# Optimization experiments

Hardware: AMD Instinct MI355X
Metric: run time of the kernel (lower is better)

## Reference

```python
import jax, jax.numpy as jnp
import numpy as np

# config dims (see shape_source)
NO = 8        # Max_Object
NT = 32       # Max_Time
C = 512       # feat_dims
VD = 1024     # visual_dim
RD = 300      # self.nfeat (relation word-vector dim)
H = 4         # headnum
B = 8         # batch
No = NT * 2 * NO      # 512 object-graph nodes
Nr = NT * NO * NO     # 2048 relation-graph nodes


def _glorot(key, shape):
    fan_in = shape[0]
    return jax.random.normal(key, shape, dtype=jnp.float32) / np.sqrt(fan_in)


def setup_inputs() -> dict:
    key = jax.random.key(0)
    ks = jax.random.split(key, 18)
    inp = {
        "Ao": jax.random.uniform(ks[0], (B, No, No), dtype=jnp.float32),
        "srco": jax.random.normal(ks[1], (B, 1, 1, No, VD), dtype=jnp.float32),
        "Ar": jax.random.uniform(ks[2], (B, Nr, Nr), dtype=jnp.float32),
        "srcr": jax.random.normal(ks[3], (B, 1, 1, Nr, RD), dtype=jnp.float32),
        # GraphConvolution weights: gcl_o/gcl2_o and gcl_r/gcl2_r
        "Wo1": _glorot(ks[4], (VD, 1024)),
        "Wo2": _glorot(ks[5], (1024, C)),
        "Wr1": _glorot(ks[6], (RD, 1024)),
        "Wr2": _glorot(ks[7], (1024, C)),
        # MultiHeadAttention (e2n) projections
        "Wq": _glorot(ks[8], (C, C)), "bq": jnp.zeros((C,), jnp.float32),
        "Wk": _glorot(ks[9], (C, C)), "bk": jnp.zeros((C,), jnp.float32),
        "Wv": _glorot(ks[10], (C, C)), "bv": jnp.zeros((C,), jnp.float32),
        "Wp": _glorot(ks[11], (C, C)), "bp": jnp.zeros((C,), jnp.float32),
        # e2n_embed: Linear(2C -> C)
        "We": _glorot(ks[12], (2 * C, C)), "be": jnp.zeros((C,), jnp.float32),
    }
    return inp


def _gcn2(A, x, W1, W2):
    """Two stacked GraphConvolution layers with self-loops: relu((A+I) @ x @ W).
    A: (b,N,N), x: (b,N,Din). Vectorized over batch (torch code loops per-sample)."""
    eye = jnp.eye(A.shape[-1], dtype=A.dtype)
    Ah = A + eye
    h = jax.nn.relu(jnp.einsum('bij,bjd->bid', Ah, x @ W1))
    return jax.nn.relu(jnp.einsum('bij,bjd->bid', Ah, h @ W2))


def _mha(x, Wq, bq, Wk, bk, Wv, bv, Wp, bp):
    """Standard multi-head self-attention. x: (Bseg, S, C)."""
    Bs, S, _ = x.shape
    dh = C // H
    q = (x @ Wq + bq).reshape(Bs, S, H, dh)
    k = (x @ Wk + bk).reshape(Bs, S, H, dh)
    v = (x @ Wv + bv).reshape(Bs, S, H, dh)
    attn = jax.nn.softmax(jnp.einsum('bqhd,bkhd->bhqk', q, k) / np.sqrt(dh), axis=-1)
    o = jnp.einsum('bhqk,bkhd->bqhd', attn, v).reshape(Bs, S, C)
    return o @ Wp + bp


def _forward(Ao, srco, Ar, srcr, Wo1, Wo2, Wr1, Wr2,
             Wq, bq, Wk, bk, Wv, bv, Wp, bp, We, be):
    b = Ao.shape[0]
    # object-graph GCN (torch loops over batch; vectorized here)
    xo = srco[:, 0, 0, :, :VD]                       # (b, No, VD)
    srco_gcn = _gcn2(Ao, xo, Wo1, Wo2)               # (b, No, C)
    out_gcn_o = srco_gcn.reshape(b, NT, 2 * NO, C)
    # relation-graph GCN
    xr = srcr[:, 0, 0]                               # (b, Nr, RD)
    srcr_gcn = _gcn2(Ar, xr, Wr1, Wr2)               # (b, Nr, C)
    out_gcn_r = srcr_gcn.reshape(b, NT, NO * NO, C)
    # compute_e2n: segment-wise MHA over NO-token windows (torch loops over NO)
    r = out_gcn_r.reshape(b * NT, NO, NO, C)
    seg_a = r.reshape(b * NT * NO, NO, C)                      # rows of NOxNO grid
    a = _mha(seg_a, Wq, bq, Wk, bk, Wv, bv, Wp, bp).mean(axis=1)
    a = a.reshape(b * NT, NO, C)
    seg_o = jnp.swapaxes(r, 1, 2).reshape(b * NT * NO, NO, C)  # cols (permute 0,2,1,3)
    o = _mha(seg_o, Wq, bq, Wk, bk, Wv, bv, Wp, bp).mean(axis=1)
    o = o.reshape(b * NT, NO, C)
    tmp = jnp.concatenate([a, o], axis=1)                      # (b*NT, 2*NO, C)
    cat = jnp.concatenate([tmp, out_gcn_o.reshape(b * NT, 2 * NO, C)], axis=-1)
    out_e2n = cat @ We + be
    return out_e2n.reshape(b, NT, 2 * NO, C)


def reference(Ao, srco, Ar, srcr, Wo1, Wo2, Wr1, Wr2,
              Wq, bq, Wk, bk, Wv, bv, Wp, bp, We, be):
    return _forward(Ao, srco, Ar, srcr, Wo1, Wo2, Wr1, Wr2,
                    Wq, bq, Wk, bk, Wv, bv, Wp, bp, We, be)
```

## Files before the change

### kernel.cpp

```cpp
#include <hip/hip_runtime.h>
#include <hip/hip_bf16.h>


typedef __attribute__((ext_vector_type(4))) float f32x4;
typedef __attribute__((ext_vector_type(8))) short bf16x8s;

#define TILE 128
#define BKK 32
#define LDSS 40

__device__ inline void splt(float v, unsigned short& h, unsigned short& l) {
    __hip_bfloat16 hb = __float2bfloat16(v);
    float hf = __bfloat162float(hb);
    __hip_bfloat16 lb = __float2bfloat16(v - hf);
    h = *(unsigned short*)&hb;
    l = *(unsigned short*)&lb;
}

__global__ __launch_bounds__(256) void gemm3p(
    const __hip_bfloat16* __restrict__ AH, const __hip_bfloat16* __restrict__ AL,
    long long sA, int lda,
    const __hip_bfloat16* __restrict__ BTH, const __hip_bfloat16* __restrict__ BTL,
    long long sBT, int ldbt,
    float* __restrict__ DF,
    __hip_bfloat16* __restrict__ DH, __hip_bfloat16* __restrict__ DL,
    long long sD, int ldd,
    const __hip_bfloat16* __restrict__ addNH, const __hip_bfloat16* __restrict__ addNL,
    long long sAddN, int ldaddN,
    const __hip_bfloat16* __restrict__ addTH, const __hip_bfloat16* __restrict__ addTL,
    long long sAddT, int ldaddT,
    const float* __restrict__ bias,
    int K, int relu)
{
    __shared__ __hip_bfloat16 Ahs[TILE * LDSS], Als[TILE * LDSS];
    __shared__ __hip_bfloat16 Bhs[TILE * LDSS], Bls[TILE * LDSS];

    const int tid  = threadIdx.x;
    const int lane = tid & 63;
    const int wave = tid >> 6;
    const int wm   = (wave >> 1) * 64;
    const int wn   = (wave & 1) * 64;
    const int row0 = blockIdx.y * TILE;
    const int col0 = blockIdx.x * TILE;
    const int b    = blockIdx.z;

    const __hip_bfloat16* AHb = AH + (size_t)b * sA;
    const __hip_bfloat16* ALb = AL + (size_t)b * sA;
    const __hip_bfloat16* BHb = BTH + (size_t)b * sBT;
    const __hip_bfloat16* BLb = BTL + (size_t)b * sBT;

    f32x4 acc[4][4];
#pragma unroll
    for (int i = 0; i < 4; ++i)
#pragma unroll
        for (int j = 0; j < 4; ++j) acc[i][j] = (f32x4){0.f, 0.f, 0.f, 0.f};

    const int quad = lane >> 4;
    const int l16  = lane & 15;

    for (int k0 = 0; k0 < K; k0 += BKK) {
        __syncthreads();
#pragma unroll
        for (int it = 0; it < 2; ++it) {
            int task = tid + it * 256;
            int m = task >> 2, kq = task & 3;
            size_t go = (size_t)(row0 + m) * lda + k0 + kq * 8;
            *(uint4*)(&Ahs[m * LDSS + kq * 8]) = *(const uint4*)(AHb + go);
            *(uint4*)(&Als[m * LDSS + kq * 8]) = *(const uint4*)(ALb + go);
        }
#pragma unroll
        for (int it = 0; it < 2; ++it) {
            int task = tid + it * 256;
            int n = task >> 2, kq = task & 3;
            size_t go = (size_t)(col0 + n) * ldbt + k0 + kq * 8;
            *(uint4*)(&Bhs[n * LDSS + kq * 8]) = *(const uint4*)(BHb + go);
            *(uint4*)(&Bls[n * LDSS + kq * 8]) = *(const uint4*)(BLb + go);
        }
        __syncthreads();

        bf16x8s ah[4], al[4], bh[4], bl[4];
#pragma unroll
        for (int mt = 0; mt < 4; ++mt) {
            int r = (wm + mt * 16 + l16) * LDSS + quad * 8;
            ah[mt] = *(const bf16x8s*)(&Ahs[r]);
            al[mt] = *(const bf16x8s*)(&Als[r]);
        }
#pragma unroll
        for (int nt = 0; nt < 4; ++nt) {
            int r = (wn + nt * 16 + l16) * LDSS + quad * 8;
            bh[nt] = *(const bf16x8s*)(&Bhs[r]);
            bl[nt] = *(const bf16x8s*)(&Bls[r]);
        }
#pragma unroll
        for (int mt = 0; mt < 4; ++mt)
#pragma unroll
            for (int nt = 0; nt < 4; ++nt) {
                acc[mt][nt] = __builtin_amdgcn_mfma_f32_16x16x32_bf16(ah[mt], bh[nt], acc[mt][nt], 0, 0, 0);
                acc[mt][nt] = __builtin_amdgcn_mfma_f32_16x16x32_bf16(ah[mt], bl[nt], acc[mt][nt], 0, 0, 0);
                acc[mt][nt] = __builtin_amdgcn_mfma_f32_16x16x32_bf16(al[mt], bh[nt], acc[mt][nt], 0, 0, 0);
            }
    }

    float* DFb = DF ? DF + (size_t)b * sD : nullptr;
    __hip_bfloat16* DHb = DH ? DH + (size_t)b * sD : nullptr;
    __hip_bfloat16* DLb = DL ? DL + (size_t)b * sD : nullptr;
    const __hip_bfloat16* aNH = addNH ? addNH + (size_t)b * sAddN : nullptr;
    const __hip_bfloat16* aNL = addNL ? addNL + (size_t)b * sAddN : nullptr;
    const __hip_bfloat16* aTH = addTH ? addTH + (size_t)b * sAddT : nullptr;
    const __hip_bfloat16* aTL = addTL ? addTL + (size_t)b * sAddT : nullptr;
#pragma unroll
    for (int mt = 0; mt < 4; ++mt)
#pragma unroll
        for (int nt = 0; nt < 4; ++nt)
#pragma unroll
            for (int r = 0; r < 4; ++r) {
                int m = row0 + wm + mt * 16 + quad * 4 + r;
                int n = col0 + wn + nt * 16 + l16;
                float v = acc[mt][nt][r];
                if (aNH) v += __bfloat162float(aNH[(size_t)m * ldaddN + n])
                            + __bfloat162float(aNL[(size_t)m * ldaddN + n]);
                if (aTH) v += __bfloat162float(aTH[(size_t)n * ldaddT + m])
                            + __bfloat162float(aTL[(size_t)n * ldaddT + m]);
                if (bias) v += bias[n];
                if (relu && v < 0.f) v = 0.f;
                if (DFb) DFb[(size_t)m * ldd + n] = v;
                else {
                    unsigned short h, l;
                    splt(v, h, l);
                    ((unsigned short*)DHb)[(size_t)m * ldd + n] = h;
                    ((unsigned short*)DLb)[(size_t)m * ldd + n] = l;
                }
            }
}

__global__ void split_planes(const float* __restrict__ src,
                             __hip_bfloat16* __restrict__ H,
                             __hip_bfloat16* __restrict__ L, int n8)
{
    int i = blockIdx.x * blockDim.x + threadIdx.x;
    if (i >= n8) return;
    float4 v0 = ((const float4*)src)[i * 2];
    float4 v1 = ((const float4*)src)[i * 2 + 1];
    float vals[8] = {v0.x, v0.y, v0.z, v0.w, v1.x, v1.y, v1.z, v1.w};
    unsigned short hh[8], ll[8];
#pragma unroll
    for (int u = 0; u < 8; ++u) splt(vals[u], hh[u], ll[u]);
    *(uint4*)((unsigned short*)H + (size_t)i * 8) = *(uint4*)hh;
    *(uint4*)((unsigned short*)L + (size_t)i * 8) = *(uint4*)ll;
}

__global__ __launch_bounds__(256) void padtrans_split(
    const float* __restrict__ src, __hip_bfloat16* __restrict__ dH,
    __hip_bfloat16* __restrict__ dL, int R, int C, int Rp, int Cp)
{
    __shared__ float T[64][65];
    const int t = threadIdx.x;
    const int tr = t >> 4, tc = t & 15;
    const int c0 = blockIdx.x * 64, r0 = blockIdx.y * 64;
    const size_t bat = blockIdx.z;
    const float* sb = src + bat * (size_t)R * C;
    unsigned short* dHb = (unsigned short*)dH + bat * (size_t)Cp * Rp;
    unsigned short* dLb = (unsigned short*)dL + bat * (size_t)Cp * Rp;

#pragma unroll
    for (int i = 0; i < 4; ++i) {
        int rr = tr + i * 16;
        int gr = r0 + rr;
        float v0 = 0.f, v1 = 0.f, v2 = 0.f, v3 = 0.f;
        if (gr < R) {
            int c = c0 + tc * 4;
            const float* s = sb + (size_t)gr * C + c;
            if (c + 0 < C) v0 = s[0];
            if (c + 1 < C) v1 = s[1];
            if (c + 2 < C) v2 = s[2];
            if (c + 3 < C) v3 = s[3];
        }
        T[rr][tc * 4 + 0] = v0; T[rr][tc * 4 + 1] = v1;
        T[rr][tc * 4 + 2] = v2; T[rr][tc * 4 + 3] = v3;
    }
    __syncthreads();
#pragma unroll
    for (int i = 0; i < 4; ++i) {
        int cc = tr + i * 16;
        unsigned short h[4], l[4];
#pragma unroll
        for (int u = 0; u < 4; ++u) splt(T[tc * 4 + u][cc], h[u], l[u]);
        size_t off = (size_t)(c0 + cc) * Rp + r0 + tc * 4;
        *(ushort4*)(dHb + off) = *(ushort4*)h;
        *(ushort4*)(dLb + off) = *(ushort4*)l;
    }
}

__global__ __launch_bounds__(256) void trans_bf16(
    const __hip_bfloat16* __restrict__ sH, const __hip_bfloat16* __restrict__ sL,
    __hip_bfloat16* __restrict__ dH, __hip_bfloat16* __restrict__ dL,
    int R, int C)
{
    __shared__ unsigned short T[64][68];
    const int plane = blockIdx.z & 1;
    const size_t bat = blockIdx.z >> 1;
    const unsigned short* s = (const unsigned short*)(plane ? sL : sH) + bat * (size_t)R * C;
    unsigned short* d = (unsigned short*)(plane ? dL : dH) + bat * (size_t)R * C;
    const int t = threadIdx.x;
    const int tr = t >> 4, tc = t & 15;
    const int c0 = blockIdx.x * 64, r0 = blockIdx.y * 64;
#pragma unroll
    for (int i = 0; i < 4; ++i) {
        int rr = tr + i * 16;
        ushort4 v = *(const ushort4*)(s + (size_t)(r0 + rr) * C + c0 + tc * 4);
        T[rr][tc * 4 + 0] = v.x; T[rr][tc * 4 + 1] = v.y;
        T[rr][tc * 4 + 2] = v.z; T[rr][tc * 4 + 3] = v.w;
    }
    __syncthreads();
#pragma unroll
    for (int i = 0; i < 4; ++i) {
        int cc = tr + i * 16;
        ushort4 o = { T[tc * 4 + 0][cc], T[tc * 4 + 1][cc],
                      T[tc * 4 + 2][cc], T[tc * 4 + 3][cc] };
        *(ushort4*)(d + (size_t)(c0 + cc) * R + r0 + tc * 4) = o;
    }
}

__global__ __launch_bounds__(256) void gemm_bf16(
    const __hip_bfloat16* __restrict__ A, long long sA, int lda,
    const __hip_bfloat16* __restrict__ B, long long sB, int ldb,
    void* __restrict__ D, long long sD, int ldd,
    const __hip_bfloat16* __restrict__ addsrc, long long sAdd, int ldadd,
    const float* __restrict__ bias,
    int K, int relu, int outF32)
{
    __shared__ __hip_bfloat16 As[TILE * LDSS];
    __shared__ __hip_bfloat16 Bs[TILE * LDSS];

    const int tid  = threadIdx.x;
    const int lane = tid & 63;
    const int wave = tid >> 6;
    const int wm   = (wave >> 1) * 64;
    const int wn   = (wave & 1) * 64;
    const int row0 = blockIdx.y * TILE;
    const int col0 = blockIdx.x * TILE;
    const int b    = blockIdx.z;

    const __hip_bfloat16* Ab = A + (size_t)b * sA;
    const __hip_bfloat16* Bb = B + (size_t)b * sB;

    f32x4 acc[4][4];
#pragma unroll
    for (int i = 0; i < 4; ++i)
#pragma unroll
        for (int j = 0; j < 4; ++j) acc[i][j] = (f32x4){0.f, 0.f, 0.f, 0.f};

    const int quad = lane >> 4;
    const int l16  = lane & 15;

    for (int k0 = 0; k0 < K; k0 += BKK) {
        __syncthreads();
#pragma unroll
        for (int it = 0; it < 2; ++it) {
            int task = tid + it * 256;
            int m = task >> 2, kq = task & 3;
            uint4 val = *(const uint4*)(Ab + (size_t)(row0 + m) * lda + k0 + kq * 8);
            *(uint4*)(&As[m * LDSS + kq * 8]) = val;
        }
#pragma unroll
        for (int it = 0; it < 2; ++it) {
            int task = tid + it * 256;
            int kk = task >> 4, n8 = task & 15;
            uint4 val = *(const uint4*)(Bb + (size_t)(k0 + kk) * ldb + col0 + n8 * 8);
            const __hip_bfloat16* v16 = (const __hip_bfloat16*)&val;
#pragma unroll
            for (int u = 0; u < 8; ++u)
                Bs[(n8 * 8 + u) * LDSS + kk] = v16[u];
        }
        __syncthreads();

        bf16x8s afrag[4], bfrag[4];
#pragma unroll
        for (int mt = 0; mt < 4; ++mt)
            afrag[mt] = *(const bf16x8s*)(&As[(wm + mt * 16 + l16) * LDSS + quad * 8]);
#pragma unroll
        for (int nt = 0; nt < 4; ++nt)
            bfrag[nt] = *(const bf16x8s*)(&Bs[(wn + nt * 16 + l16) * LDSS + quad * 8]);
#pragma unroll
        for (int mt = 0; mt < 4; ++mt)
#pragma unroll
            for (int nt = 0; nt < 4; ++nt)
                acc[mt][nt] = __builtin_amdgcn_mfma_f32_16x16x32_bf16(
                    afrag[mt], bfrag[nt], acc[mt][nt], 0, 0, 0);
    }

    __hip_bfloat16* Db16 = (__hip_bfloat16*)D + (size_t)b * sD;
    float*          DbF  = (float*)D + (size_t)b * sD;
    const __hip_bfloat16* Addb = addsrc ? addsrc + (size_t)b * sAdd : nullptr;
#pragma unroll
    for (int mt = 0; mt < 4; ++mt)
#pragma unroll
        for (int nt = 0; nt < 4; ++nt)
#pragma unroll
            for (int r = 0; r < 4; ++r) {
                int m = row0 + wm + mt * 16 + quad * 4 + r;
                int n = col0 + wn + nt * 16 + l16;
                float v = acc[mt][nt][r];
                if (Addb) v += __bfloat162float(Addb[(size_t)m * ldadd + n]);
                if (bias) v += bias[n];
                if (relu && v < 0.f) v = 0.f;
                if (outF32) DbF[(size_t)m * ldd + n] = v;
                else        Db16[(size_t)m * ldd + n] = __float2bfloat16(v);
            }
}

__global__ void convert_kernel(const float* __restrict__ src,
                               __hip_bfloat16* __restrict__ dst, int n4)
{
    int i = blockIdx.x * blockDim.x + threadIdx.x;
    if (i >= n4) return;
    float4 v = ((const float4*)src)[i];
    __hip_bfloat16 t0 = __float2bfloat16(v.x), t1 = __float2bfloat16(v.y);
    __hip_bfloat16 t2 = __float2bfloat16(v.z), t3 = __float2bfloat16(v.w);
    ushort4 o = { *(unsigned short*)&t0, *(unsigned short*)&t1,
                  *(unsigned short*)&t2, *(unsigned short*)&t3 };
    ((ushort4*)dst)[i] = o;
}

__global__ __launch_bounds__(256) void attn_kernel(
    const float* __restrict__ q,
    const float* __restrict__ k,
    const float* __restrict__ v,
    __hip_bfloat16* __restrict__ abar)
{
    __shared__ float qs[8][512], ks[8][512], vs[8][512];
    __shared__ float sc[4][8][8];
    __shared__ float wb[4][8];

    const int tid  = threadIdx.x;
    const int mode = blockIdx.y;
    const int g    = blockIdx.x >> 3;
    const int idx  = blockIdx.x & 7;
    const int rowBase = g * 64;

    for (int t = tid; t < 512; t += 256) {
        int p = t >> 6, c8 = (t & 63) * 8;
        int row = (mode == 0) ? (rowBase + idx * 8 + p) : (rowBase + p * 8 + idx);
        const float* qp = q + (size_t)row * 512 + c8;
        const float* kp = k + (size_t)row * 512 + c8;
        const float* vp = v + (size_t)row * 512 + c8;
        *(float4*)(&qs[p][c8])     = *(const float4*)(qp);
        *(float4*)(&qs[p][c8 + 4]) = *(const float4*)(qp + 4);
        *(float4*)(&ks[p][c8])     = *(const float4*)(kp);
        *(float4*)(&ks[p][c8 + 4]) = *(const float4*)(kp + 4);
        *(float4*)(&vs[p][c8])     = *(const float4*)(vp);
        *(float4*)(&vs[p][c8 + 4]) = *(const float4*)(vp + 4);
    }
    __syncthreads();

    {
        int h = tid >> 6, l = tid & 63;
        int i = l >> 3, j = l & 7;
        const float* qrow = &qs[i][h * 128];
        const float* krow = &ks[j][h * 128];
        float s = 0.f;
#pragma unroll
        for (int d = 0; d < 128; d += 4) {
            float4 qa = *(const float4*)(qrow + d);
            float4 kb = *(const float4*)(krow + d);
            s += qa.x * kb.x + qa.y * kb.y + qa.z * kb.z + qa.w * kb.w;
        }
        sc[h][i][j] = s * 0.08838834764831845f;
    }
    __syncthreads();

    if (tid < 32) {
        int h = tid >> 3, i = tid & 7;
        float mx = -1e30f;
#pragma unroll
        for (int j = 0; j < 8; ++j) mx = fmaxf(mx, sc[h][i][j]);
        float e[8], sum = 0.f;
#pragma unroll
        for (int j = 0; j < 8; ++j) { e[j] = __expf(sc[h][i][j] - mx); sum += e[j]; }
        float inv = 1.f / sum;
#pragma unroll
        for (int j = 0; j < 8; ++j) sc[h][i][j] = e[j] * inv;
    }
    __syncthreads();

    if (tid < 32) {
        int h = tid >> 3, j = tid & 7;
        float s = 0.f;
#pragma unroll
        for (int i = 0; i < 8; ++i) s += sc[h][i][j];
        wb[h][j] = s * 0.125f;
    }
    __syncthreads();

    {
        int orow = g * 16 + mode * 8 + idx;
        for (int c = tid; c < 512; c += 256) {
            int h = c >> 7;
            float o = 0.f;
#pragma unroll
            for (int j = 0; j < 8; ++j) o += wb[h][j] * vs[j][c];
            abar[(size_t)orow * 512 + c] = __float2bfloat16(o);
        }
    }
}


extern "C" void kernel_launch(void* const* d_in, const int* in_sizes, int n_in,
                              void* d_out, int out_size, void* d_ws, size_t ws_size,
                              hipStream_t stream)
{
    const float* Ao   = (const float*)d_in[0];
    const float* srco = (const float*)d_in[1];
    const float* Ar   = (const float*)d_in[2];
    const float* srcr = (const float*)d_in[3];
    const float* Wo1  = (const float*)d_in[4];
    const float* Wo2  = (const float*)d_in[5];
    const float* Wr1  = (const float*)d_in[6];
    const float* Wr2  = (const float*)d_in[7];
    const float* Wq   = (const float*)d_in[8];
    const float* bq   = (const float*)d_in[9];
    const float* Wk   = (const float*)d_in[10];
    const float* bk   = (const float*)d_in[11];
    const float* Wv   = (const float*)d_in[12];
    const float* bv   = (const float*)d_in[13];
    const float* Wp   = (const float*)d_in[14];
    const float* bp   = (const float*)d_in[15];
    const float* We   = (const float*)d_in[16];
    const float* be   = (const float*)d_in[17];
    float* out = (float*)d_out;

    char* ws = (char*)d_ws;
    __hip_bfloat16* ArH   = (__hip_bfloat16*)(ws + 0);
    __hip_bfloat16* ArL   = (__hip_bfloat16*)(ws + 67108864);
    __hip_bfloat16* XPTH  = (__hip_bfloat16*)(ws + 134217728);
    __hip_bfloat16* XPTL  = (__hip_bfloat16*)(ws + 146800640);
    __hip_bfloat16* UH    = (__hip_bfloat16*)(ws + 159383552);
    __hip_bfloat16* UL    = (__hip_bfloat16*)(ws + 171966464);
    __hip_bfloat16* HRH   = (__hip_bfloat16*)(ws + 184549376);
    __hip_bfloat16* HRL   = (__hip_bfloat16*)(ws + 218103808);
    __hip_bfloat16* T2RH  = (__hip_bfloat16*)(ws + 134217728);
    __hip_bfloat16* T2RL  = (__hip_bfloat16*)(ws + 150994944);
    __hip_bfloat16* T2RTH = (__hip_bfloat16*)(ws + 167772160);
    __hip_bfloat16* T2RTL = (__hip_bfloat16*)(ws + 184549376);
    __hip_bfloat16* GRH   = (__hip_bfloat16*)(ws + 201326592);
    __hip_bfloat16* GRL   = (__hip_bfloat16*)(ws + 218103808);
    float* qF = (float*)(ws + 0);
    float* kF = (float*)(ws + 33554432);
    float* vF = (float*)(ws + 67108864);
    __hip_bfloat16* ABAR  = (__hip_bfloat16*)(ws + 100663296);
    __hip_bfloat16* TO    = (__hip_bfloat16*)(ws + 104857600);
    __hip_bfloat16* HO    = (__hip_bfloat16*)(ws + 113246208);
    __hip_bfloat16* T2O   = (__hip_bfloat16*)(ws + 121634816);
    __hip_bfloat16* CAT   = (__hip_bfloat16*)(ws + 125829120);
    __hip_bfloat16* srcoB = (__hip_bfloat16*)(ws + 134217728);
    __hip_bfloat16* AoB   = (__hip_bfloat16*)(ws + 142606336);
    __hip_bfloat16* Wo1B  = (__hip_bfloat16*)(ws + 146800640);
    __hip_bfloat16* Wo2B  = (__hip_bfloat16*)(ws + 148897792);
    __hip_bfloat16* WeB   = (__hip_bfloat16*)(ws + 149946368);
    __hip_bfloat16* WpB   = (__hip_bfloat16*)(ws + 150994944);
    __hip_bfloat16* WPTH  = (__hip_bfloat16*)(ws + 251658240);
    __hip_bfloat16* WPTL  = (__hip_bfloat16*)(ws + 252313600);
    __hip_bfloat16* Wr2TH = (__hip_bfloat16*)(ws + 252968960);
    __hip_bfloat16* Wr2TL = (__hip_bfloat16*)(ws + 254017536);
    __hip_bfloat16* WqTH  = (__hip_bfloat16*)(ws + 255066112);
    __hip_bfloat16* WqTL  = (__hip_bfloat16*)(ws + 255590400);
    __hip_bfloat16* WkTH  = (__hip_bfloat16*)(ws + 256114688);
    __hip_bfloat16* WkTL  = (__hip_bfloat16*)(ws + 256638976);
    __hip_bfloat16* WvB   = (__hip_bfloat16*)(ws + 257163264);

    dim3 blk(256);
    auto cvt = [&](const float* s, __hip_bfloat16* d, int n) {
        convert_kernel<<<dim3((n / 4 + 255) / 256), blk, 0, stream>>>(s, d, n / 4);
    };

    split_planes<<<dim3(33554432 / 8 / 256), blk, 0, stream>>>(Ar, ArH, ArL, 33554432 / 8);
    padtrans_split<<<dim3(6, 32, 8), blk, 0, stream>>>(srcr, XPTH, XPTL, 2048, 300, 2048, 384);
    padtrans_split<<<dim3(16, 5, 1), blk, 0, stream>>>(Wr1, WPTH, WPTL, 300, 1024, 320, 1024);
    padtrans_split<<<dim3(8, 16, 1), blk, 0, stream>>>(Wr2, Wr2TH, Wr2TL, 1024, 512, 1024, 512);
    padtrans_split<<<dim3(8, 8, 1), blk, 0, stream>>>(Wq, WqTH, WqTL, 512, 512, 512, 512);
    padtrans_split<<<dim3(8, 8, 1), blk, 0, stream>>>(Wk, WkTH, WkTL, 512, 512, 512, 512);
    cvt(Wv, WvB, 262144);

    gemm3p<<<dim3(3, 16, 8), blk, 0, stream>>>(
        ArH, ArL, 2048LL * 2048, 2048, XPTH, XPTL, 384LL * 2048, 2048,
        nullptr, UH, UL, 2048LL * 384, 384,
        nullptr, nullptr, 0, 0, XPTH, XPTL, 384LL * 2048, 2048,
        nullptr, 2048, 0);
    gemm3p<<<dim3(8, 128, 1), blk, 0, stream>>>(
        UH, UL, 0, 384, WPTH, WPTL, 0, 320,
        nullptr, HRH, HRL, 0, 1024,
        nullptr, nullptr, 0, 0, nullptr, nullptr, 0, 0,
        nullptr, 320, 1);
    gemm3p<<<dim3(4, 128, 1), blk, 0, stream>>>(
        HRH, HRL, 0, 1024, Wr2TH, Wr2TL, 0, 1024,
        nullptr, T2RH, T2RL, 0, 512,
        nullptr, nullptr, 0, 0, nullptr, nullptr, 0, 0,
        nullptr, 1024, 0);
    trans_bf16<<<dim3(8, 32, 16), blk, 0, stream>>>(T2RH, T2RL, T2RTH, T2RTL, 2048, 512);
    gemm3p<<<dim3(4, 16, 8), blk, 0, stream>>>(
        ArH, ArL, 2048LL * 2048, 2048, T2RTH, T2RTL, 512LL * 2048, 2048,
        nullptr, GRH, GRL, 2048LL * 512, 512,
        T2RH, T2RL, 2048LL * 512, 512, nullptr, nullptr, 0, 0,
        nullptr, 2048, 1);
    gemm3p<<<dim3(4, 128, 1), blk, 0, stream>>>(
        GRH, GRL, 0, 512, WqTH, WqTL, 0, 512,
        qF, nullptr, nullptr, 0, 512,
        nullptr, nullptr, 0, 0, nullptr, nullptr, 0, 0,
        bq, 512, 0);
    gemm3p<<<dim3(4, 128, 1), blk, 0, stream>>>(
        GRH, GRL, 0, 512, WkTH, WkTL, 0, 512,
        kF, nullptr, nullptr, 0, 512,
        nullptr, nullptr, 0, 0, nullptr, nullptr, 0, 0,
        bk, 512, 0);
    gemm_bf16<<<dim3(4, 128, 1), blk, 0, stream>>>(
        GRH, 0, 512, WvB, 0, 512, vF, 0, 512,
        nullptr, 0, 0, bv, 512, 0, 1);
    attn_kernel<<<dim3(2048, 2), blk, 0, stream>>>(qF, kF, vF, ABAR);

    cvt(srco, srcoB, 4194304);
    cvt(Ao, AoB, 2097152);
    cvt(Wo1, Wo1B, 1048576);
    cvt(Wo2, Wo2B, 524288);
    cvt(We, WeB, 524288);
    cvt(Wp, WpB, 262144);
    gemm_bf16<<<dim3(8, 32, 1), blk, 0, stream>>>(srcoB, 0, 1024, Wo1B, 0, 1024,
        TO, 0, 1024, nullptr, 0, 0, nullptr, 1024, 0, 0);
    gemm_bf16<<<dim3(8, 4, 8), blk, 0, stream>>>(AoB, 512LL * 512, 512, TO, 512LL * 1024, 1024,
        HO, 512LL * 1024, 1024, TO, 512LL * 1024, 1024, nullptr, 512, 1, 0);
    gemm_bf16<<<dim3(4, 32, 1), blk, 0, stream>>>(HO, 0, 1024, Wo2B, 0, 512,
        T2O, 0, 512, nullptr, 0, 0, nullptr, 1024, 0, 0);
    gemm_bf16<<<dim3(4, 4, 8), blk, 0, stream>>>(AoB, 512LL * 512, 512, T2O, 512LL * 512, 512,
        (void*)(CAT + 512), 512LL * 1024, 1024, T2O, 512LL * 512, 512, nullptr, 512, 1, 0);
    gemm_bf16<<<dim3(4, 32, 1), blk, 0, stream>>>(ABAR, 0, 512, WpB, 0, 512,
        CAT, 0, 1024, nullptr, 0, 0, bp, 512, 0, 0);
    gemm_bf16<<<dim3(4, 32, 1), blk, 0, stream>>>(CAT, 0, 1024, WeB, 0, 512,
        out, 0, 512, nullptr, 0, 0, be, 1024, 0, 1);
}
```

Measured before the change: 1.258 ms.

## Double-buffer LDS tiles in GEMM kernels and fuse Q/K projections

Both GEMM kernels now use two LDS buffers and prefetch the next K-slice from global memory into registers while the current slice's MFMAs run, leaving one barrier per iteration instead of two. Separately, the Q and K projection weights are packed into one 1024-wide transposed matrix, so a single gemm3p launch writes an interleaved QK buffer using a per-column bias select, and the attention kernel reads Q and K from that buffer. The cost is doubled LDS use, which may lower occupancy, and more live registers for the prefetch.

```diff
diff --git a/kernel.cpp b/kernel.cpp
--- a/kernel.cpp
+++ b/kernel.cpp
@@ -29,11 +29,11 @@
     long long sAddN, int ldaddN,
     const __hip_bfloat16* __restrict__ addTH, const __hip_bfloat16* __restrict__ addTL,
     long long sAddT, int ldaddT,
-    const float* __restrict__ bias,
+    const float* __restrict__ bias, const float* __restrict__ bias2, int nsplit,
     int K, int relu)
 {
-    __shared__ __hip_bfloat16 Ahs[TILE * LDSS], Als[TILE * LDSS];
-    __shared__ __hip_bfloat16 Bhs[TILE * LDSS], Bls[TILE * LDSS];
+    __shared__ __hip_bfloat16 Ahs[2][TILE * LDSS], Als[2][TILE * LDSS];
+    __shared__ __hip_bfloat16 Bhs[2][TILE * LDSS], Bls[2][TILE * LDSS];
 
     const int tid  = threadIdx.x;
     const int lane = tid & 63;
@@ -49,6 +49,9 @@
     const __hip_bfloat16* BHb = BTH + (size_t)b * sBT;
     const __hip_bfloat16* BLb = BTL + (size_t)b * sBT;
 
+    const int mA  = tid >> 2;
+    const int kqA = (tid & 3) * 8;
+
     f32x4 acc[4][4];
 #pragma unroll
     for (int i = 0; i < 4; ++i)
@@ -58,38 +61,50 @@
     const int quad = lane >> 4;
     const int l16  = lane & 15;
 
+    {
+#pragma unroll
+        for (int it = 0; it < 2; ++it) {
+            int m = mA + it * 64;
+            size_t goA = (size_t)(row0 + m) * lda + kqA;
+            size_t goB = (size_t)(col0 + m) * ldbt + kqA;
+            int lo = m * LDSS + kqA;
+            *(uint4*)(&Ahs[0][lo]) = *(const uint4*)(AHb + goA);
+            *(uint4*)(&Als[0][lo]) = *(const uint4*)(ALb + goA);
+            *(uint4*)(&Bhs[0][lo]) = *(const uint4*)(BHb + goB);
+            *(uint4*)(&Bls[0][lo]) = *(const uint4*)(BLb + goB);
+        }
+    }
+    __syncthreads();
+
+    int cur = 0;
     for (int k0 = 0; k0 < K; k0 += BKK) {
-        __syncthreads();
-#pragma unroll
-        for (int it = 0; it < 2; ++it) {
-            int task = tid + it * 256;
-            int m = task >> 2, kq = task & 3;
-            size_t go = (size_t)(row0 + m) * lda + k0 + kq * 8;
-            *(uint4*)(&Ahs[m * LDSS + kq * 8]) = *(const uint4*)(AHb + go);
-            *(uint4*)(&Als[m * LDSS + kq * 8]) = *(const uint4*)(ALb + go);
-        }
-#pragma unroll
-        for (int it = 0; it < 2; ++it) {
-            int task = tid + it * 256;
-            int n = task >> 2, kq = task & 3;
-            size_t go = (size_t)(col0 + n) * ldbt + k0 + kq * 8;
-            *(uint4*)(&Bhs[n * LDSS + kq * 8]) = *(const uint4*)(BHb + go);
-            *(uint4*)(&Bls[n * LDSS + kq * 8]) = *(const uint4*)(BLb + go);
-        }
-        __syncthreads();
+        const bool pf = (k0 + BKK) < K;
+        uint4 rAH[2], rAL[2], rBH[2], rBL[2];
+        if (pf) {
+#pragma unroll
+            for (int it = 0; it < 2; ++it) {
+                int m = mA + it * 64;
+                size_t goA = (size_t)(row0 + m) * lda + (k0 + BKK) + kqA;
+                size_t goB = (size_t)(col0 + m) * ldbt + (k0 + BKK) + kqA;
+                rAH[it] = *(const uint4*)(AHb + goA);
+                rAL[it] = *(const uint4*)(ALb + goA);
+                rBH[it] = *(const uint4*)(BHb + goB);
+                rBL[it] = *(const uint4*)(BLb + goB);
+            }
+        }
 
         bf16x8s ah[4], al[4], bh[4], bl[4];
 #pragma unroll
         for (int mt = 0; mt < 4; ++mt) {
             int r = (wm + mt * 16 + l16) * LDSS + quad * 8;
-            ah[mt] = *(const bf16x8s*)(&Ahs[r]);
-            al[mt] = *(const bf16x8s*)(&Als[r]);
+            ah[mt] = *(const bf16x8s*)(&Ahs[cur][r]);
+            al[mt] = *(const bf16x8s*)(&Als[cur][r]);
         }
 #pragma unroll
         for (int nt = 0; nt < 4; ++nt) {
             int r = (wn + nt * 16 + l16) * LDSS + quad * 8;
-            bh[nt] = *(const bf16x8s*)(&Bhs[r]);
-            bl[nt] = *(const bf16x8s*)(&Bls[r]);
+            bh[nt] = *(const bf16x8s*)(&Bhs[cur][r]);
+            bl[nt] = *(const bf16x8s*)(&Bls[cur][r]);
         }
 #pragma unroll
         for (int mt = 0; mt < 4; ++mt)
@@ -99,6 +114,21 @@
                 acc[mt][nt] = __builtin_amdgcn_mfma_f32_16x16x32_bf16(ah[mt], bl[nt], acc[mt][nt], 0, 0, 0);
                 acc[mt][nt] = __builtin_amdgcn_mfma_f32_16x16x32_bf16(al[mt], bh[nt], acc[mt][nt], 0, 0, 0);
             }
+
+        if (pf) {
+            int nxt = cur ^ 1;
+#pragma unroll
+            for (int it = 0; it < 2; ++it) {
+                int m = mA + it * 64;
+                int lo = m * LDSS + kqA;
+                *(uint4*)(&Ahs[nxt][lo]) = rAH[it];
+                *(uint4*)(&Als[nxt][lo]) = rAL[it];
+                *(uint4*)(&Bhs[nxt][lo]) = rBH[it];
+                *(uint4*)(&Bls[nxt][lo]) = rBL[it];
+            }
+        }
+        __syncthreads();
+        cur ^= 1;
     }
 
     float* DFb = DF ? DF + (size_t)b * sD : nullptr;
@@ -121,7 +151,7 @@
                             + __bfloat162float(aNL[(size_t)m * ldaddN + n]);
                 if (aTH) v += __bfloat162float(aTH[(size_t)n * ldaddT + m])
                             + __bfloat162float(aTL[(size_t)n * ldaddT + m]);
-                if (bias) v += bias[n];
+                if (bias) v += (bias2 && n >= nsplit) ? bias2[n - nsplit] : bias[n];
                 if (relu && v < 0.f) v = 0.f;
                 if (DFb) DFb[(size_t)m * ldd + n] = v;
                 else {
@@ -229,8 +259,8 @@
     const float* __restrict__ bias,
     int K, int relu, int outF32)
 {
-    __shared__ __hip_bfloat16 As[TILE * LDSS];
-    __shared__ __hip_bfloat16 Bs[TILE * LDSS];
+    __shared__ __hip_bfloat16 As[2][TILE * LDSS];
+    __shared__ __hip_bfloat16 Bs[2][TILE * LDSS];
 
     const int tid  = threadIdx.x;
     const int lane = tid & 63;
@@ -244,6 +274,11 @@
     const __hip_bfloat16* Ab = A + (size_t)b * sA;
     const __hip_bfloat16* Bb = B + (size_t)b * sB;
 
+    const int mA  = tid >> 2;
+    const int kqA = (tid & 3) * 8;
+    const int kkB = tid >> 4;
+    const int n8B = (tid & 15) * 8;
+
     f32x4 acc[4][4];
 #pragma unroll
     for (int i = 0; i < 4; ++i)
@@ -253,40 +288,65 @@
     const int quad = lane >> 4;
     const int l16  = lane & 15;
 
+    {
+#pragma unroll
+        for (int it = 0; it < 2; ++it) {
+            int m = mA + it * 64;
+            *(uint4*)(&As[0][m * LDSS + kqA]) =
+                *(const uint4*)(Ab + (size_t)(row0 + m) * lda + kqA);
+            int kk = kkB + it * 16;
+            uint4 val = *(const uint4*)(Bb + (size_t)kk * ldb + col0 + n8B);
+            const __hip_bfloat16* v16 = (const __hip_bfloat16*)&val;
+#pragma unroll
+            for (int u = 0; u < 8; ++u)
+                Bs[0][(n8B + u) * LDSS + kk] = v16[u];
+        }
+    }
+    __syncthreads();
+
+    int cur = 0;
     for (int k0 = 0; k0 < K; k0 += BKK) {
-        __syncthreads();
-#pragma unroll
-        for (int it = 0; it < 2; ++it) {
-            int task = tid + it * 256;
-            int m = task >> 2, kq = task & 3;
-            uint4 val = *(const uint4*)(Ab + (size_t)(row0 + m) * lda + k0 + kq * 8);
-            *(uint4*)(&As[m * LDSS + kq * 8]) = val;
-        }
-#pragma unroll
-        for (int it = 0; it < 2; ++it) {
-            int task = tid + it * 256;
-            int kk = task >> 4, n8 = task & 15;
-            uint4 val = *(const uint4*)(Bb + (size_t)(k0 + kk) * ldb + col0 + n8 * 8);
-            const __hip_bfloat16* v16 = (const __hip_bfloat16*)&val;
-#pragma unroll
-            for (int u = 0; u < 8; ++u)
-                Bs[(n8 * 8 + u) * LDSS + kk] = v16[u];
-        }
-        __syncthreads();
+        const bool pf = (k0 + BKK) < K;
+        uint4 rA[2], rB[2];
+        if (pf) {
+#pragma unroll
+            for (int it = 0; it < 2; ++it) {
+                int m = mA + it * 64;
+                rA[it] = *(const uint4*)(Ab + (size_t)(row0 + m) * lda + (k0 + BKK) + kqA);
+                int kk = kkB + it * 16;
+                rB[it] = *(const uint4*)(Bb + (size_t)(k0 + BKK + kk) * ldb + col0 + n8B);
+            }
+        }
 
         bf16x8s afrag[4], bfrag[4];
 #pragma unroll
         for (int mt = 0; mt < 4; ++mt)
-            afrag[mt] = *(const bf16x8s*)(&As[(wm + mt * 16 + l16) * LDSS + quad * 8]);
+            afrag[mt] = *(const bf16x8s*)(&As[cur][(wm + mt * 16 + l16) * LDSS + quad * 8]);
 #pragma unroll
         for (int nt = 0; nt < 4; ++nt)
-            bfrag[nt] = *(const bf16x8s*)(&Bs[(wn + nt * 16 + l16) * LDSS + quad * 8]);
+            bfrag[nt] = *(const bf16x8s*)(&Bs[cur][(wn + nt * 16 + l16) * LDSS + quad * 8]);
 #pragma unroll
         for (int mt = 0; mt < 4; ++mt)
 #pragma unroll
             for (int nt = 0; nt < 4; ++nt)
                 acc[mt][nt] = __builtin_amdgcn_mfma_f32_16x16x32_bf16(
                     afrag[mt], bfrag[nt], acc[mt][nt], 0, 0, 0);
+
+        if (pf) {
+            int nxt = cur ^ 1;
+#pragma unroll
+            for (int it = 0; it < 2; ++it) {
+                int m = mA + it * 64;
+                *(uint4*)(&As[nxt][m * LDSS + kqA]) = rA[it];
+                int kk = kkB + it * 16;
+                const __hip_bfloat16* v16 = (const __hip_bfloat16*)&rB[it];
+#pragma unroll
+                for (int u = 0; u < 8; ++u)
+                    Bs[nxt][(n8B + u) * LDSS + kk] = v16[u];
+            }
+        }
+        __syncthreads();
+        cur ^= 1;
     }
 
     __hip_bfloat16* Db16 = (__hip_bfloat16*)D + (size_t)b * sD;
@@ -323,8 +383,7 @@
 }
 
 __global__ __launch_bounds__(256) void attn_kernel(
-    const float* __restrict__ q,
-    const float* __restrict__ k,
+    const float* __restrict__ qk,
     const float* __restrict__ v,
     __hip_bfloat16* __restrict__ abar)
 {
@@ -341,8 +400,8 @@
     for (int t = tid; t < 512; t += 256) {
         int p = t >> 6, c8 = (t & 63) * 8;
         int row = (mode == 0) ? (rowBase + idx * 8 + p) : (rowBase + p * 8 + idx);
-        const float* qp = q + (size_t)row * 512 + c8;
-        const float* kp = k + (size_t)row * 512 + c8;
+        const float* qp = qk + (size_t)row * 1024 + c8;
+        const float* kp = qp + 512;
         const float* vp = v + (size_t)row * 512 + c8;
         *(float4*)(&qs[p][c8])     = *(const float4*)(qp);
         *(float4*)(&qs[p][c8 + 4]) = *(const float4*)(qp + 4);
@@ -444,9 +503,8 @@
     __hip_bfloat16* T2RTL = (__hip_bfloat16*)(ws + 184549376);
     __hip_bfloat16* GRH   = (__hip_bfloat16*)(ws + 201326592);
     __hip_bfloat16* GRL   = (__hip_bfloat16*)(ws + 218103808);
-    float* qF = (float*)(ws + 0);
-    float* kF = (float*)(ws + 33554432);
-    float* vF = (float*)(ws + 67108864);
+    float* qkF = (float*)(ws + 0);
+    float* vF  = (float*)(ws + 67108864);
     __hip_bfloat16* ABAR  = (__hip_bfloat16*)(ws + 100663296);
     __hip_bfloat16* TO    = (__hip_bfloat16*)(ws + 104857600);
     __hip_bfloat16* HO    = (__hip_bfloat16*)(ws + 113246208);
@@ -462,10 +520,8 @@
     __hip_bfloat16* WPTL  = (__hip_bfloat16*)(ws + 252313600);
     __hip_bfloat16* Wr2TH = (__hip_bfloat16*)(ws + 252968960);
     __hip_bfloat16* Wr2TL = (__hip_bfloat16*)(ws + 254017536);
-    __hip_bfloat16* WqTH  = (__hip_bfloat16*)(ws + 255066112);
-    __hip_bfloat16* WqTL  = (__hip_bfloat16*)(ws + 255590400);
-    __hip_bfloat16* WkTH  = (__hip_bfloat16*)(ws + 256114688);
-    __hip_bfloat16* WkTL  = (__hip_bfloat16*)(ws + 256638976);
+    __hip_bfloat16* WqkTH = (__hip_bfloat16*)(ws + 255066112);
+    __hip_bfloat16* WqkTL = (__hip_bfloat16*)(ws + 256114688);
     __hip_bfloat16* WvB   = (__hip_bfloat16*)(ws + 257163264);
 
     dim3 blk(256);
@@ -477,45 +533,41 @@
     padtrans_split<<<dim3(6, 32, 8), blk, 0, stream>>>(srcr, XPTH, XPTL, 2048, 300, 2048, 384);
     padtrans_split<<<dim3(16, 5, 1), blk, 0, stream>>>(Wr1, WPTH, WPTL, 300, 1024, 320, 1024);
     padtrans_split<<<dim3(8, 16, 1), blk, 0, stream>>>(Wr2, Wr2TH, Wr2TL, 1024, 512, 1024, 512);
-    padtrans_split<<<dim3(8, 8, 1), blk, 0, stream>>>(Wq, WqTH, WqTL, 512, 512, 512, 512);
-    padtrans_split<<<dim3(8, 8, 1), blk, 0, stream>>>(Wk, WkTH, WkTL, 512, 512, 512, 512);
+    padtrans_split<<<dim3(8, 8, 1), blk, 0, stream>>>(Wq, WqkTH, WqkTL, 512, 512, 512, 512);
+    padtrans_split<<<dim3(8, 8, 1), blk, 0, stream>>>(Wk, WqkTH + 262144, WqkTL + 262144,
+                                                      512, 512, 512, 512);
     cvt(Wv, WvB, 262144);
 
     gemm3p<<<dim3(3, 16, 8), blk, 0, stream>>>(
         ArH, ArL, 2048LL * 2048, 2048, XPTH, XPTL, 384LL * 2048, 2048,
         nullptr, UH, UL, 2048LL * 384, 384,
         nullptr, nullptr, 0, 0, XPTH, XPTL, 384LL * 2048, 2048,
-        nullptr, 2048, 0);
+        nullptr, nullptr, 0, 2048, 0);
     gemm3p<<<dim3(8, 128, 1), blk, 0, stream>>>(
         UH, UL, 0, 384, WPTH, WPTL, 0, 320,
         nullptr, HRH, HRL, 0, 1024,
         nullptr, nullptr, 0, 0, nullptr, nullptr, 0, 0,
-        nullptr, 320, 1);
+        nullptr, nullptr, 0, 320, 1);
     gemm3p<<<dim3(4, 128, 1), blk, 0, stream>>>(
         HRH, HRL, 0, 1024, Wr2TH, Wr2TL, 0, 1024,
         nullptr, T2RH, T2RL, 0, 512,
         nullptr, nullptr, 0, 0, nullptr, nullptr, 0, 0,
-        nullptr, 1024, 0);
+        nullptr, nullptr, 0, 1024, 0);
     trans_bf16<<<dim3(8, 32, 16), blk, 0, stream>>>(T2RH, T2RL, T2RTH, T2RTL, 2048, 512);
     gemm3p<<<dim3(4, 16, 8), blk, 0, stream>>>(
         ArH, ArL, 2048LL * 2048, 2048, T2RTH, T2RTL, 512LL * 2048, 2048,
         nullptr, GRH, GRL, 2048LL * 512, 512,
         T2RH, T2RL, 2048LL * 512, 512, nullptr, nullptr, 0, 0,
-        nullptr, 2048, 1);
-    gemm3p<<<dim3(4, 128, 1), blk, 0, stream>>>(
-        GRH, GRL, 0, 512, WqTH, WqTL, 0, 512,
-        qF, nullptr, nullptr, 0, 512,
+        nullptr, nullptr, 0, 2048, 1);
+    gemm3p<<<dim3(8, 128, 1), blk, 0, stream>>>(
+        GRH, GRL, 0, 512, WqkTH, WqkTL, 0, 512,
+        qkF, nullptr, nullptr, 0, 1024,
         nullptr, nullptr, 0, 0, nullptr, nullptr, 0, 0,
-        bq, 512, 0);
-    gemm3p<<<dim3(4, 128, 1), blk, 0, stream>>>(
-        GRH, GRL, 0, 512, WkTH, WkTL, 0, 512,
-        kF, nullptr, nullptr, 0, 512,
-        nullptr, nullptr, 0, 0, nullptr, nullptr, 0, 0,
-        bk, 512, 0);
+        bq, bk, 512, 512, 0);
     gemm_bf16<<<dim3(4, 128, 1), blk, 0, stream>>>(
         GRH, 0, 512, WvB, 0, 512, vF, 0, 512,
         nullptr, 0, 0, bv, 512, 0, 1);
-    attn_kernel<<<dim3(2048, 2), blk, 0, stream>>>(qF, kF, vF, ABAR);
+    attn_kernel<<<dim3(2048, 2), blk, 0, stream>>>(qkF, vF, ABAR);
 
     cvt(srco, srcoB, 4194304);
     cvt(Ao, AoB, 2097152);
```

Measured after the change: 2.105 ms. +67.3%, slower.
